# Performance work log

Measured on AMD Instinct MI355X. Metric: run time of the kernel, lower is better.

The kernel has to match this reference:

```python
import jax, jax.numpy as jnp
import numpy as np

SIGMA = 0.1
SIG2 = SIGMA * SIGMA  # sigma^2


def _gauss_conv(x, y, b):
    # x: BxNxD, y: BxKxD, b: BxKxd -> BxNxd
    # K_ij = exp(-||x_i - y_j||^2 / (2 sigma^2)); out_i = sum_j K_ij b_j
    d2 = jnp.sum((x[:, :, None, :] - y[:, None, :, :]) ** 2, axis=-1)  # BxNxK
    K = jnp.exp(-d2 / (2.0 * SIG2))
    return jnp.einsum('bnk,bkd->bnd', K, b)


def _gauss_grad(p, x):
    # grad-of-kernel N-body sum (py=px=p, y=x as in grad_kernel(mom, pos)):
    # out_i = sum_j <p_i, p_j> * grad_{x_i} K(x_i, x_j)
    #       = sum_j <p_i, p_j> * K_ij * (-(x_i - x_j) / sigma^2)
    diff = x[:, :, None, :] - x[:, None, :, :]            # BxNxKxD
    d2 = jnp.sum(diff ** 2, axis=-1)                      # BxNxK
    K = jnp.exp(-d2 / (2.0 * SIG2))
    C = jnp.einsum('bnd,bkd->bnk', p, p)                  # <p_i, p_j>
    return jnp.einsum('bnk,bnkd->bnd', -(K * C) / SIG2, diff)


def setup_inputs() -> dict:
    key = jax.random.key(0)
    k1, k2 = jax.random.split(key)
    B, N, D = 1, 8192, 3
    mom = jax.random.normal(k1, (B, N, D), dtype=jnp.float32)
    pos = jax.random.normal(k2, (B, N, D), dtype=jnp.float32)
    return {"mom": mom, "pos": pos}


def reference(mom, pos):
    # variational_evolve: (dmom/dt, dpos/dt) = (-grad_kernel(mom,pos), kernel(pos,pos,mom))
    dmom = -_gauss_grad(mom, pos)
    dpos = _gauss_conv(pos, pos, mom)
    return (dmom, dpos)
```

## Files before the change

### kernel.cpp

```cpp
#include <hip/hip_runtime.h>


#define NPTS  8192
#define NCXY  16
#define NCZ   32
#define NCELL (NCXY * NCXY * NCZ)
#define ORIGIN    (-4.0f)
#define EDGE      0.5f
#define INV_EDGE  2.0f
#define INV_EDGEZ 4.0f
#define RCUT2     0.25f

#define A_DOT 144.269504088896f
#define A_R   (-72.134752044448f)
#define INV_SIG2 100.0f

#define EXP2(x) __builtin_amdgcn_exp2f(x)

__device__ __forceinline__ int clampi(int c, int hi) { return min(max(c, 0), hi); }

__device__ __forceinline__ int cell_of(float x, float y, float z) {
    const int cx = clampi((int)floorf((x - ORIGIN) * INV_EDGE),  NCXY - 1);
    const int cy = clampi((int)floorf((y - ORIGIN) * INV_EDGE),  NCXY - 1);
    const int cz = clampi((int)floorf((z - ORIGIN) * INV_EDGEZ), NCZ  - 1);
    return (cx * NCXY + cy) * NCZ + cz;
}

__global__ __launch_bounds__(1024)
void k_countscan(const float* __restrict__ pos,
                 int* __restrict__ start, int* __restrict__ cur)
{
    __shared__ int cnt[NCELL];
    __shared__ int wtot[16];
    __shared__ int wexcl[16];
    const int t = threadIdx.x;
    const int lane = t & 63;
    const int wid = t >> 6;

    #pragma unroll
    for (int k = 0; k < NCELL / 1024; ++k) cnt[t + k * 1024] = 0;
    __syncthreads();

    #pragma unroll
    for (int k = 0; k < NPTS / 1024; ++k) {
        const int i = t + k * 1024;
        atomicAdd(&cnt[cell_of(pos[3*i+0], pos[3*i+1], pos[3*i+2])], 1);
    }
    __syncthreads();

    int pre[8];
    int s = 0;
    #pragma unroll
    for (int k = 0; k < 8; ++k) { pre[k] = s; s += cnt[8*t + k]; }
    int p = s;
    #pragma unroll
    for (int off = 1; off < 64; off <<= 1) {
        const int v = __shfl_up(p, off);
        if (lane >= off) p += v;
    }
    if (lane == 63) wtot[wid] = p;
    __syncthreads();
    if (t < 16) {
        const int w = wtot[t];
        int q = w;
        #pragma unroll
        for (int off = 1; off < 16; off <<= 1) {
            const int v = __shfl_up(q, off);
            if (t >= off) q += v;
        }
        wexcl[t] = q - w;
    }
    __syncthreads();
    const int base = wexcl[wid] + (p - s);
    #pragma unroll
    for (int k = 0; k < 8; ++k) {
        const int v = base + pre[k];
        start[8*t + k] = v;
        cur[8*t + k] = v;
    }
    if (t == 0) start[NCELL] = NPTS;
}

__global__ __launch_bounds__(256)
void k_scatter(const float* __restrict__ mom, const float* __restrict__ pos,
               int* __restrict__ cur,
               float* __restrict__ pmP, float* __restrict__ pmM,
               int* __restrict__ inv)
{
    const int i = blockIdx.x * 256 + threadIdx.x;
    const float x = pos[3*i+0], y = pos[3*i+1], z = pos[3*i+2];
    const int dst = atomicAdd(&cur[cell_of(x, y, z)], 1);
    const float r2 = x*x + y*y + z*z;
    reinterpret_cast<float4*>(pmP)[dst] = make_float4(A_DOT*x, A_DOT*y, A_DOT*z, A_R*r2);
    reinterpret_cast<float4*>(pmM)[dst] = make_float4(mom[3*i+0], mom[3*i+1], mom[3*i+2], 0.0f);
    inv[dst] = i;
}

__global__ __launch_bounds__(256)
void k_main(const float* __restrict__ mom, const float* __restrict__ pos,
            const float* __restrict__ pmP, const float* __restrict__ pmM,
            const int* __restrict__ inv, const int* __restrict__ start,
            float* __restrict__ out)
{
    const int wid  = (blockIdx.x * 256 + threadIdx.x) >> 6;
    const int lane = threadIdx.x & 63;

    const int oi = inv[wid];
    const float xi = pos[3*oi+0], yi = pos[3*oi+1], zi = pos[3*oi+2];
    const float pxi = mom[3*oi+0], pyi = mom[3*oi+1], pzi = mom[3*oi+2];
    const float ci  = A_R * (xi*xi + yi*yi + zi*zi);

    const int cx = clampi((int)floorf((xi - ORIGIN) * INV_EDGE), NCXY - 1);
    const int cy = clampi((int)floorf((yi - ORIGIN) * INV_EDGE), NCXY - 1);

    int st_l = 0, len_l = 0;
    if (lane < 9) {
        const int nx = cx + (lane / 3) - 1;
        const int ny = cy + (lane % 3) - 1;
        if (nx >= 0 && nx < NCXY && ny >= 0 && ny < NCXY) {
            const float X0 = ORIGIN + nx * EDGE;
            const float Y0 = ORIGIN + ny * EDGE;
            const float dx = fmaxf(fmaxf(X0 - xi, xi - (X0 + EDGE)), 0.0f);
            const float dy = fmaxf(fmaxf(Y0 - yi, yi - (Y0 + EDGE)), 0.0f);
            const float m2 = dx * dx + dy * dy;
            if (m2 <= RCUT2) {
                const float zr = __builtin_sqrtf(RCUT2 - m2);
                const int z0 = clampi((int)floorf((zi - zr - ORIGIN) * INV_EDGEZ), NCZ - 1);
                const int z1 = clampi((int)floorf((zi + zr - ORIGIN) * INV_EDGEZ), NCZ - 1);
                const int base = (nx * NCXY + ny) * NCZ;
                st_l  = start[base + z0];
                len_l = start[base + z1 + 1] - st_l;
            }
        }
    }

    int pref = len_l;
    #pragma unroll
    for (int off = 1; off < 16; off <<= 1) {
        const int v = __shfl_up(pref, off);
        if (lane >= off) pref += v;
    }
    const int T = __shfl(pref, 8);

    int p0[9], ofs[9];
    #pragma unroll
    for (int q = 0; q < 9; ++q) {
        const int pr = __shfl(pref, q);
        const int ln = __shfl(len_l, q);
        const int st = __shfl(st_l, q);
        p0[q]  = pr - ln;
        ofs[q] = st - (pr - ln);
    }

    float S = 0.f, SPx = 0.f, SPy = 0.f, SPz = 0.f;
    float apx = 0.f, apy = 0.f, apz = 0.f;

    const float4* __restrict__ pmPv = reinterpret_cast<const float4*>(pmP);
    const float4* __restrict__ pmMv = reinterpret_cast<const float4*>(pmM);

    for (int f0 = 0; f0 < T; f0 += 64) {
        const int f = f0 + lane;
        int off_sel = ofs[0];
        #pragma unroll
        for (int q = 1; q < 9; ++q)
            off_sel = (f >= p0[q]) ? ofs[q] : off_sel;
        if (f < T) {
            const int j = f + off_sel;
            const float4 P = pmPv[j];
            const float4 M = pmMv[j];
            float arg = __builtin_fmaf(zi, P.z, ci + P.w);
            arg = __builtin_fmaf(yi, P.y, arg);
            arg = __builtin_fmaf(xi, P.x, arg);
            const float K = EXP2(arg);
            const float C = __builtin_fmaf(pzi, M.z,
                              __builtin_fmaf(pyi, M.y, pxi * M.x));
            const float s = K * C;
            S += s;
            SPx = __builtin_fmaf(s, P.x, SPx);
            SPy = __builtin_fmaf(s, P.y, SPy);
            SPz = __builtin_fmaf(s, P.z, SPz);
            apx = __builtin_fmaf(K, M.x, apx);
            apy = __builtin_fmaf(K, M.y, apy);
            apz = __builtin_fmaf(K, M.z, apz);
        }
    }

    #pragma unroll
    for (int off = 1; off < 64; off <<= 1) {
        S   += __shfl_xor(S,   off);
        SPx += __shfl_xor(SPx, off);
        SPy += __shfl_xor(SPy, off);
        SPz += __shfl_xor(SPz, off);
        apx += __shfl_xor(apx, off);
        apy += __shfl_xor(apy, off);
        apz += __shfl_xor(apz, off);
    }

    if (lane == 0) {
        const float us = INV_SIG2 / A_DOT;
        out[3*oi+0] = INV_SIG2 * xi * S - us * SPx;
        out[3*oi+1] = INV_SIG2 * yi * S - us * SPy;
        out[3*oi+2] = INV_SIG2 * zi * S - us * SPz;
        out[3*NPTS + 3*oi+0] = apx;
        out[3*NPTS + 3*oi+1] = apy;
        out[3*NPTS + 3*oi+2] = apz;
    }
}

extern "C" void kernel_launch(void* const* d_in, const int* in_sizes, int n_in,
                              void* d_out, int out_size, void* d_ws, size_t ws_size,
                              hipStream_t stream)
{
    const float* mom = (const float*)d_in[0];
    const float* pos = (const float*)d_in[1];
    float* out = (float*)d_out;

    float* pmP  = (float*)d_ws;
    float* pmM  = pmP + (size_t)4 * NPTS;
    int* inv    = (int*)(pmM + (size_t)4 * NPTS);
    int* start  = inv + NPTS;
    int* cur    = start + NCELL + 1;

    k_countscan<<<1, 1024, 0, stream>>>(pos, start, cur);
    k_scatter<<<NPTS / 256, 256, 0, stream>>>(mom, pos, cur, pmP, pmM, inv);
    k_main<<<(NPTS * 64) / 256, 256, 0, stream>>>(mom, pos, pmP, pmM, inv, start, out);
}
```

Baseline: 23.94 us.

## Fuse cell count, scan and scatter into one single-block prep kernel

Merges the counting/scan kernel and the scatter kernel into one single-block kernel. Each point's rank inside its cell is kept from the shared-memory atomic and added to the scanned cell start, which removes a kernel launch and the global atomics on the cursor array. The main kernel now reads each query point from the sorted float4 buffers by its own wave index instead of gathering through inv, and reads inv only at output time. The cost is that the scatter work now runs in a single 1024-thread block rather than across 32 blocks, and xi/yi/zi are recovered by dividing out a scale factor, which can shift the last bits.

```diff
diff --git a/kernel.cpp b/kernel.cpp
--- a/kernel.cpp
+++ b/kernel.cpp
@@ -12,6 +12,7 @@
 #define RCUT2     0.25f
 
 #define A_DOT 144.269504088896f
+#define INV_ADOT (1.0f / 144.269504088896f)
 #define A_R   (-72.134752044448f)
 #define INV_SIG2 100.0f
 
@@ -27,8 +28,10 @@
 }
 
 __global__ __launch_bounds__(1024)
-void k_countscan(const float* __restrict__ pos,
-                 int* __restrict__ start, int* __restrict__ cur)
+void k_prep(const float* __restrict__ mom, const float* __restrict__ pos,
+            int* __restrict__ start,
+            float* __restrict__ pmP, float* __restrict__ pmM,
+            int* __restrict__ inv)
 {
     __shared__ int cnt[NCELL];
     __shared__ int wtot[16];
@@ -41,10 +44,12 @@
     for (int k = 0; k < NCELL / 1024; ++k) cnt[t + k * 1024] = 0;
     __syncthreads();
 
-    #pragma unroll
-    for (int k = 0; k < NPTS / 1024; ++k) {
+    int cid[8], rnk[8];
+    #pragma unroll
+    for (int k = 0; k < 8; ++k) {
         const int i = t + k * 1024;
-        atomicAdd(&cnt[cell_of(pos[3*i+0], pos[3*i+1], pos[3*i+2])], 1);
+        cid[k] = cell_of(pos[3*i+0], pos[3*i+1], pos[3*i+2]);
+        rnk[k] = atomicAdd(&cnt[cid[k]], 1);
     }
     __syncthreads();
 
@@ -76,39 +81,43 @@
     for (int k = 0; k < 8; ++k) {
         const int v = base + pre[k];
         start[8*t + k] = v;
-        cur[8*t + k] = v;
     }
     if (t == 0) start[NCELL] = NPTS;
+    __syncthreads();
+    #pragma unroll
+    for (int k = 0; k < 8; ++k) cnt[8*t + k] = base + pre[k];
+    __syncthreads();
+
+    #pragma unroll
+    for (int k = 0; k < 8; ++k) {
+        const int i = t + k * 1024;
+        const int dst = cnt[cid[k]] + rnk[k];
+        const float x = pos[3*i+0], y = pos[3*i+1], z = pos[3*i+2];
+        const float r2 = x*x + y*y + z*z;
+        reinterpret_cast<float4*>(pmP)[dst] =
+            make_float4(A_DOT*x, A_DOT*y, A_DOT*z, A_R*r2);
+        reinterpret_cast<float4*>(pmM)[dst] =
+            make_float4(mom[3*i+0], mom[3*i+1], mom[3*i+2], 0.0f);
+        inv[dst] = i;
+    }
 }
 
 __global__ __launch_bounds__(256)
-void k_scatter(const float* __restrict__ mom, const float* __restrict__ pos,
-               int* __restrict__ cur,
-               float* __restrict__ pmP, float* __restrict__ pmM,
-               int* __restrict__ inv)
-{
-    const int i = blockIdx.x * 256 + threadIdx.x;
-    const float x = pos[3*i+0], y = pos[3*i+1], z = pos[3*i+2];
-    const int dst = atomicAdd(&cur[cell_of(x, y, z)], 1);
-    const float r2 = x*x + y*y + z*z;
-    reinterpret_cast<float4*>(pmP)[dst] = make_float4(A_DOT*x, A_DOT*y, A_DOT*z, A_R*r2);
-    reinterpret_cast<float4*>(pmM)[dst] = make_float4(mom[3*i+0], mom[3*i+1], mom[3*i+2], 0.0f);
-    inv[dst] = i;
-}
-
-__global__ __launch_bounds__(256)
-void k_main(const float* __restrict__ mom, const float* __restrict__ pos,
-            const float* __restrict__ pmP, const float* __restrict__ pmM,
+void k_main(const float* __restrict__ pmP, const float* __restrict__ pmM,
             const int* __restrict__ inv, const int* __restrict__ start,
             float* __restrict__ out)
 {
     const int wid  = (blockIdx.x * 256 + threadIdx.x) >> 6;
     const int lane = threadIdx.x & 63;
 
-    const int oi = inv[wid];
-    const float xi = pos[3*oi+0], yi = pos[3*oi+1], zi = pos[3*oi+2];
-    const float pxi = mom[3*oi+0], pyi = mom[3*oi+1], pzi = mom[3*oi+2];
-    const float ci  = A_R * (xi*xi + yi*yi + zi*zi);
+    const float4* __restrict__ pmPv = reinterpret_cast<const float4*>(pmP);
+    const float4* __restrict__ pmMv = reinterpret_cast<const float4*>(pmM);
+
+    const float4 Pi = pmPv[wid];
+    const float4 Mi = pmMv[wid];
+    const float xi = Pi.x * INV_ADOT, yi = Pi.y * INV_ADOT, zi = Pi.z * INV_ADOT;
+    const float pxi = Mi.x, pyi = Mi.y, pzi = Mi.z;
+    const float ci  = Pi.w;
 
     const int cx = clampi((int)floorf((xi - ORIGIN) * INV_EDGE), NCXY - 1);
     const int cy = clampi((int)floorf((yi - ORIGIN) * INV_EDGE), NCXY - 1);
@@ -154,9 +163,6 @@
 
     float S = 0.f, SPx = 0.f, SPy = 0.f, SPz = 0.f;
     float apx = 0.f, apy = 0.f, apz = 0.f;
-
-    const float4* __restrict__ pmPv = reinterpret_cast<const float4*>(pmP);
-    const float4* __restrict__ pmMv = reinterpret_cast<const float4*>(pmM);
 
     for (int f0 = 0; f0 < T; f0 += 64) {
         const int f = f0 + lane;
@@ -197,6 +203,7 @@
     }
 
     if (lane == 0) {
+        const int oi = inv[wid];
         const float us = INV_SIG2 / A_DOT;
         out[3*oi+0] = INV_SIG2 * xi * S - us * SPx;
         out[3*oi+1] = INV_SIG2 * yi * S - us * SPy;
@@ -219,9 +226,7 @@
     float* pmM  = pmP + (size_t)4 * NPTS;
     int* inv    = (int*)(pmM + (size_t)4 * NPTS);
     int* start  = inv + NPTS;
-    int* cur    = start + NCELL + 1;
-
-    k_countscan<<<1, 1024, 0, stream>>>(pos, start, cur);
-    k_scatter<<<NPTS / 256, 256, 0, stream>>>(mom, pos, cur, pmP, pmM, inv);
-    k_main<<<(NPTS * 64) / 256, 256, 0, stream>>>(mom, pos, pmP, pmM, inv, start, out);
-}
+
+    k_prep<<<1, 1024, 0, stream>>>(mom, pos, start, pmP, pmM, inv);
+    k_main<<<(NPTS * 64) / 256, 256, 0, stream>>>(pmP, pmM, inv, start, out);
+}
```

Measured after the change: 34.90 us. 1.46x slower.

## Process two particles per wavefront with 32-lane groups and swizzled order

Applied to the files above, without the earlier changes.

k_main now assigns two sorted particles to each 64-lane wavefront, one per 32-lane half, which halves the number of wavefronts launched. Each target reads its own data from the sorted float4 buffers instead of gathering pos/mom through inv, and a bit-swizzled index spreads neighbouring cells across blocks. The goal is to cut underused lanes on short neighbour lists and to cut per-wave setup cost. In exchange, each wave loops to the longer of its two lists, so one half can sit idle, and the inner loop takes twice as many iterations per particle.

```diff
diff --git a/kernel.cpp b/kernel.cpp
--- a/kernel.cpp
+++ b/kernel.cpp
@@ -12,6 +12,7 @@
 #define RCUT2     0.25f
 
 #define A_DOT 144.269504088896f
+#define INV_ADOT (1.0f / 144.269504088896f)
 #define A_R   (-72.134752044448f)
 #define INV_SIG2 100.0f
 
@@ -97,26 +98,34 @@
 }
 
 __global__ __launch_bounds__(256)
-void k_main(const float* __restrict__ mom, const float* __restrict__ pos,
-            const float* __restrict__ pmP, const float* __restrict__ pmM,
+void k_main(const float* __restrict__ pmP, const float* __restrict__ pmM,
             const int* __restrict__ inv, const int* __restrict__ start,
             float* __restrict__ out)
 {
-    const int wid  = (blockIdx.x * 256 + threadIdx.x) >> 6;
-    const int lane = threadIdx.x & 63;
-
-    const int oi = inv[wid];
-    const float xi = pos[3*oi+0], yi = pos[3*oi+1], zi = pos[3*oi+2];
-    const float pxi = mom[3*oi+0], pyi = mom[3*oi+1], pzi = mom[3*oi+2];
-    const float ci  = A_R * (xi*xi + yi*yi + zi*zi);
+    const int w     = (blockIdx.x * 256 + threadIdx.x) >> 6;
+    const int lane  = threadIdx.x & 63;
+    const int glane = lane & 31;
+    const int grp   = lane >> 5;
+
+    const int v  = ((w & 255) << 4) | (w >> 8);
+    const int si = 2 * v + grp;
+
+    const float4* __restrict__ pmPv = reinterpret_cast<const float4*>(pmP);
+    const float4* __restrict__ pmMv = reinterpret_cast<const float4*>(pmM);
+
+    const float4 Pi = pmPv[si];
+    const float4 Mi = pmMv[si];
+    const float xi = Pi.x * INV_ADOT, yi = Pi.y * INV_ADOT, zi = Pi.z * INV_ADOT;
+    const float pxi = Mi.x, pyi = Mi.y, pzi = Mi.z;
+    const float ci  = Pi.w;
 
     const int cx = clampi((int)floorf((xi - ORIGIN) * INV_EDGE), NCXY - 1);
     const int cy = clampi((int)floorf((yi - ORIGIN) * INV_EDGE), NCXY - 1);
 
     int st_l = 0, len_l = 0;
-    if (lane < 9) {
-        const int nx = cx + (lane / 3) - 1;
-        const int ny = cy + (lane % 3) - 1;
+    if (glane < 9) {
+        const int nx = cx + (glane / 3) - 1;
+        const int ny = cy + (glane % 3) - 1;
         if (nx >= 0 && nx < NCXY && ny >= 0 && ny < NCXY) {
             const float X0 = ORIGIN + nx * EDGE;
             const float Y0 = ORIGIN + ny * EDGE;
@@ -137,17 +146,19 @@
     int pref = len_l;
     #pragma unroll
     for (int off = 1; off < 16; off <<= 1) {
-        const int v = __shfl_up(pref, off);
-        if (lane >= off) pref += v;
-    }
-    const int T = __shfl(pref, 8);
+        const int vv = __shfl_up(pref, off);
+        if (glane >= off) pref += vv;
+    }
+    const int gbase = lane & 32;
+    const int T = __shfl(pref, gbase + 8);
+    const int Tmax = max(__shfl(pref, 8), __shfl(pref, 40));
 
     int p0[9], ofs[9];
     #pragma unroll
     for (int q = 0; q < 9; ++q) {
-        const int pr = __shfl(pref, q);
-        const int ln = __shfl(len_l, q);
-        const int st = __shfl(st_l, q);
+        const int pr = __shfl(pref, gbase + q);
+        const int ln = __shfl(len_l, gbase + q);
+        const int st = __shfl(st_l, gbase + q);
         p0[q]  = pr - ln;
         ofs[q] = st - (pr - ln);
     }
@@ -155,11 +166,8 @@
     float S = 0.f, SPx = 0.f, SPy = 0.f, SPz = 0.f;
     float apx = 0.f, apy = 0.f, apz = 0.f;
 
-    const float4* __restrict__ pmPv = reinterpret_cast<const float4*>(pmP);
-    const float4* __restrict__ pmMv = reinterpret_cast<const float4*>(pmM);
-
-    for (int f0 = 0; f0 < T; f0 += 64) {
-        const int f = f0 + lane;
+    for (int f0 = 0; f0 < Tmax; f0 += 32) {
+        const int f = f0 + glane;
         int off_sel = ofs[0];
         #pragma unroll
         for (int q = 1; q < 9; ++q)
@@ -186,7 +194,7 @@
     }
 
     #pragma unroll
-    for (int off = 1; off < 64; off <<= 1) {
+    for (int off = 1; off < 32; off <<= 1) {
         S   += __shfl_xor(S,   off);
         SPx += __shfl_xor(SPx, off);
         SPy += __shfl_xor(SPy, off);
@@ -196,7 +204,8 @@
         apz += __shfl_xor(apz, off);
     }
 
-    if (lane == 0) {
+    if (glane == 0) {
+        const int oi = inv[si];
         const float us = INV_SIG2 / A_DOT;
         out[3*oi+0] = INV_SIG2 * xi * S - us * SPx;
         out[3*oi+1] = INV_SIG2 * yi * S - us * SPy;
@@ -223,5 +232,5 @@
 
     k_countscan<<<1, 1024, 0, stream>>>(pos, start, cur);
     k_scatter<<<NPTS / 256, 256, 0, stream>>>(mom, pos, cur, pmP, pmM, inv);
-    k_main<<<(NPTS * 64) / 256, 256, 0, stream>>>(mom, pos, pmP, pmM, inv, start, out);
-}
+    k_main<<<1024, 256, 0, stream>>>(pmP, pmM, inv, start, out);
+}
```

After: 27.77 us. 1.16x slower.
